# Optimization experiments

Measured on AMD Instinct MI355X. Metric: run time of the kernel, lower is better.

Reference implementation:

```python
import jax, jax.numpy as jnp
import numpy as np

ETA = 1.0
C_STAB = 0.1
SIGMA2 = 512.0  # RBF bandwidth, kernel_args['sigma2']
N_SAMPLE, S, D = 8192, 64, 512


def rbf_kernel(x, sigma2):
    # K[i,j] = exp(-||x_i - x_j||^2 / (2*sigma2)); x: [n, d] -> K: [n, n]
    sq = jnp.sum(x * x, axis=1)
    d2 = sq[:, None] + sq[None, :] - 2.0 * (x @ x.T)
    return jnp.exp(-d2 / (2.0 * sigma2))


def setup_inputs() -> dict:
    key = jax.random.key(0)
    k1, k2, k3 = jax.random.split(key, 3)
    return {
        "input_data": jax.random.normal(k1, (N_SAMPLE, D), dtype=jnp.float32),
        "weight": jax.random.normal(k2, (N_SAMPLE, S), dtype=jnp.float32),
        "inv_lambda_diag": jax.random.normal(k3, (S,), dtype=jnp.float32),
    }


def reference(input_data, weight, inv_lambda_diag):
    K = rbf_kernel(input_data, SIGMA2)          # [n, n]
    E = weight.T @ K                             # [s, n] : e_j for all samples at once
    # loss1 = sum_i e_i^T diag(inv_lambda) e_i, scaled
    loss1 = -jnp.sum(inv_lambda_diag[:, None] * E * E) / (2.0 * ETA ** 2)
    # loss2 = trace(W^T K W) = sum_{s,n} E[s,n] * W[n,s]
    loss2 = jnp.einsum("sn,ns->", E, weight) / (2.0 * ETA)
    L = loss1 + loss2
    return L + (C_STAB / 2.0) * jnp.square(L)
```

## Files before the change

kernel.cpp:

```cpp
#include <hip/hip_runtime.h>
#include <hip/hip_bf16.h>

typedef __bf16 bf16x8 __attribute__((ext_vector_type(8)));
typedef float f32x4 __attribute__((ext_vector_type(4)));
typedef long longx2 __attribute__((ext_vector_type(2)));

#define N 8192
#define D 512
#define NS 64

#define XS_OFF 0
#define WT_OFF (4 * 1024 * 1024)
#define SQ_OFF (WT_OFF + 1024 * 1024)
#define E_OFF  (SQ_OFF + 32 * 1024)
#define SC_OFF (E_OFF + N * NS * 4)

__global__ __launch_bounds__(256) void prep_x(const float* __restrict__ X,
                                              unsigned char* __restrict__ Xs,
                                              float* __restrict__ sq) {
    int row = blockIdx.x * 4 + (threadIdx.x >> 6);
    int l = threadIdx.x & 63;
    const float* src = X + (size_t)row * D + l * 8;
    float4 v0 = *(const float4*)src;
    float4 v1 = *(const float4*)(src + 4);
    int w0 = __builtin_amdgcn_cvt_pk_fp8_f32(v0.x, v0.y, 0, false);
    w0     = __builtin_amdgcn_cvt_pk_fp8_f32(v0.z, v0.w, w0, true);
    int w1 = __builtin_amdgcn_cvt_pk_fp8_f32(v1.x, v1.y, 0, false);
    w1     = __builtin_amdgcn_cvt_pk_fp8_f32(v1.z, v1.w, w1, true);
    int g = l >> 3, kh = (l >> 2) & 1, q = l & 3;
    int pos = g * 64 + ((q ^ (row & 3)) << 4) + (kh << 3);
    uint2 pk = make_uint2((unsigned)w0, (unsigned)w1);
    *(uint2*)(Xs + (size_t)row * 512 + pos) = pk;
    float acc = v0.x*v0.x + v0.y*v0.y + v0.z*v0.z + v0.w*v0.w
              + v1.x*v1.x + v1.y*v1.y + v1.z*v1.z + v1.w*v1.w;
    for (int off = 32; off > 0; off >>= 1) acc += __shfl_down(acc, off);
    if (l == 0) sq[row] = acc;
}

__global__ __launch_bounds__(256) void prep_w(const float* __restrict__ W,
                                              __bf16* __restrict__ WTs) {
    __shared__ float T[64][65];
    int i0 = blockIdx.x * 64;
    int t = threadIdx.x;
    for (int j = 0; j < 16; ++j) {
        int idx = t + 256 * j;
        int r = idx >> 6;
        int c = idx & 63;
        T[c][r] = W[(size_t)(i0 + r) * NS + c];
    }
    __syncthreads();
    for (int h = 0; h < 2; ++h)
        for (int j = 0; j < 8; ++j) {
            int idx = t + 256 * j;
            int s = idx >> 5, il = idx & 31;
            WTs[(size_t)(blockIdx.x * 2 + h) * 2048 + idx] = (__bf16)T[s][h * 32 + il];
        }
}

__global__ __launch_bounds__(256, 2) void kpca_main(
        const unsigned char* __restrict__ Xs, const __bf16* __restrict__ WTs,
        const float* __restrict__ sq, float* __restrict__ Eg) {
    __shared__ __align__(16) unsigned char U[34816];
    __shared__ __align__(16) __bf16 WT[8192];
    __shared__ __align__(16) float sqI[128];

    unsigned char* Xi = U;
    unsigned char* Xn = U + 8192;
    __bf16* KT = (__bf16*)U;

    const int t = threadIdx.x;
    const int w = t >> 6, l = t & 63;
    const int quad = l >> 4, l15 = l & 15;
    const int wm = w >> 1, wn = w & 1;
    const int n0 = blockIdx.x * 128;
    const int ic0 = blockIdx.y * 1024;
    const int fro = (quad ^ (l15 & 3)) << 4;

    float sqn_v[4];
    for (int nt = 0; nt < 4; ++nt)
        sqn_v[nt] = sq[n0 + wn * 64 + nt * 16 + l15];

    f32x4 accE[4][2];
    for (int st = 0; st < 4; ++st)
        for (int n2 = 0; n2 < 2; ++n2)
            accE[st][n2] = (f32x4){0.f, 0.f, 0.f, 0.f};

    const int c0 = t, c1 = t + 256;
    const int r0 = c0 >> 2, b0 = (c0 & 3) * 16;
    const int r1 = c1 >> 2, b1 = (c1 & 3) * 16;

    for (int it = 0; it < 8; ++it) {
        const int i0 = ic0 + it * 128;

        uint4 wv[4];
        const char* wb = (const char*)(WTs + (size_t)(i0 >> 5) * 2048);
        for (int j = 0; j < 4; ++j)
            wv[j] = *(const uint4*)(wb + (t + 256 * j) * 16);
        __syncthreads();
        for (int j = 0; j < 4; ++j)
            *(uint4*)((char*)WT + (t + 256 * j) * 16) = wv[j];
        if (t < 128) sqI[t] = sq[i0 + t];

        f32x4 accG[4][4];
        for (int mt = 0; mt < 4; ++mt)
            for (int nt = 0; nt < 4; ++nt)
                accG[mt][nt] = (f32x4){0.f, 0.f, 0.f, 0.f};

        for (int kc8 = 0; kc8 < 8; ++kc8) {
            const int kc = kc8 * 64;
            uint4 xi0 = *(const uint4*)(Xs + (size_t)(i0 + r0) * 512 + kc + b0);
            uint4 xi1 = *(const uint4*)(Xs + (size_t)(i0 + r1) * 512 + kc + b1);
            uint4 xn0 = *(const uint4*)(Xs + (size_t)(n0 + r0) * 512 + kc + b0);
            uint4 xn1 = *(const uint4*)(Xs + (size_t)(n0 + r1) * 512 + kc + b1);
            if (kc8) __syncthreads();
            *(uint4*)(Xi + c0 * 16) = xi0;
            *(uint4*)(Xi + c1 * 16) = xi1;
            *(uint4*)(Xn + c0 * 16) = xn0;
            *(uint4*)(Xn + c1 * 16) = xn1;
            __syncthreads();
            longx2 a[4], b[4];
            for (int mt = 0; mt < 4; ++mt)
                a[mt] = *(const longx2*)(Xi + (wm * 64 + mt * 16 + l15) * 64 + fro);
            for (int nt = 0; nt < 4; ++nt)
                b[nt] = *(const longx2*)(Xn + (wn * 64 + nt * 16 + l15) * 64 + fro);
            for (int mt = 0; mt < 4; ++mt)
                for (int nt = 0; nt < 4; ++nt)
                    accG[mt][nt] = __builtin_amdgcn_mfma_f32_16x16x32_fp8_fp8(
                        a[mt][0], b[nt][0], accG[mt][nt], 0, 0, 0);
            for (int mt = 0; mt < 4; ++mt)
                for (int nt = 0; nt < 4; ++nt)
                    accG[mt][nt] = __builtin_amdgcn_mfma_f32_16x16x32_fp8_fp8(
                        a[mt][1], b[nt][1], accG[mt][nt], 0, 0, 0);
        }
        __syncthreads();

        for (int mt = 0; mt < 4; ++mt) {
            int ibase = wm * 64 + mt * 16 + quad * 4;
            f32x4 si = *(const f32x4*)&sqI[ibase];
            for (int nt = 0; nt < 4; ++nt) {
                int nloc = wn * 64 + nt * 16 + l15;
                float sn = sqn_v[nt];
                union { __bf16 h[4]; uint2 u; } pk;
                for (int r = 0; r < 4; ++r) {
                    float d2 = si[r] + sn - 2.0f * accG[mt][nt][r];
                    pk.h[r] = (__bf16)__expf(d2 * -9.765625e-4f);
                }
                *(uint2*)(KT + nloc * 136 + ibase) = pk.u;
            }
        }
        __syncthreads();

        for (int kc2 = 0; kc2 < 4; ++kc2) {
            bf16x8 aw[4], bk[2];
            for (int st = 0; st < 4; ++st)
                aw[st] = *(const bf16x8*)(WT + kc2 * 2048 + (st * 16 + l15) * 32 + quad * 8);
            for (int n2 = 0; n2 < 2; ++n2)
                bk[n2] = *(const bf16x8*)(KT + (w * 32 + n2 * 16 + l15) * 136 + kc2 * 32 + quad * 8);
            for (int st = 0; st < 4; ++st)
                for (int n2 = 0; n2 < 2; ++n2)
                    accE[st][n2] = __builtin_amdgcn_mfma_f32_16x16x32_bf16(
                        aw[st], bk[n2], accE[st][n2], 0, 0, 0);
        }
    }

    for (int st = 0; st < 4; ++st)
        for (int n2 = 0; n2 < 2; ++n2)
            for (int r = 0; r < 4; ++r) {
                int s = st * 16 + quad * 4 + r;
                int n = n0 + w * 32 + n2 * 16 + l15;
                atomicAdd(Eg + (size_t)s * N + n, accE[st][n2][r]);
            }
}

__global__ __launch_bounds__(256) void loss_kernel(const float* __restrict__ Eg,
                                                   const float* __restrict__ W,
                                                   const float* __restrict__ lam,
                                                   float* __restrict__ Sacc) {
    int s = blockIdx.x;
    int t = threadIdx.x;
    float a1 = 0.f, a2 = 0.f;
    for (int n = t; n < N; n += 256) {
        float e = Eg[(size_t)s * N + n];
        a1 += e * e;
        a2 += e * W[(size_t)n * NS + s];
    }
    for (int off = 32; off > 0; off >>= 1) {
        a1 += __shfl_down(a1, off);
        a2 += __shfl_down(a2, off);
    }
    __shared__ float r1[4], r2[4];
    int wv = t >> 6, ln = t & 63;
    if (ln == 0) { r1[wv] = a1; r2[wv] = a2; }
    __syncthreads();
    if (t == 0) {
        atomicAdd(Sacc + 0, lam[s] * (r1[0] + r1[1] + r1[2] + r1[3]));
        atomicAdd(Sacc + 1, r2[0] + r2[1] + r2[2] + r2[3]);
    }
}

__global__ void finalize(const float* __restrict__ Sacc, float* __restrict__ out) {
    float L = 0.5f * (Sacc[1] - Sacc[0]);
    out[0] = L + 0.05f * L * L;
}

extern "C" void kernel_launch(void* const* d_in, const int* in_sizes, int n_in,
                              void* d_out, int out_size, void* d_ws, size_t ws_size,
                              hipStream_t stream) {
    const float* X   = (const float*)d_in[0];
    const float* W   = (const float*)d_in[1];
    const float* lam = (const float*)d_in[2];
    float* out = (float*)d_out;
    char* ws = (char*)d_ws;
    unsigned char* Xs = (unsigned char*)(ws + XS_OFF);
    __bf16* WTs = (__bf16*)(ws + WT_OFF);
    float* sq   = (float*)(ws + SQ_OFF);
    float* Eg   = (float*)(ws + E_OFF);
    float* Sacc = (float*)(ws + SC_OFF);

    hipMemsetAsync(Eg, 0, (size_t)N * NS * 4 + 8, stream);
    prep_x<<<N / 4, 256, 0, stream>>>(X, Xs, sq);
    prep_w<<<N / 64, 256, 0, stream>>>(W, WTs);
    kpca_main<<<dim3(64, 8), 256, 0, stream>>>(Xs, WTs, sq, Eg);
    loss_kernel<<<NS, 256, 0, stream>>>(Eg, W, lam, Sacc);
    finalize<<<1, 1, 0, stream>>>(Sacc, out);
}
```

Baseline: 178.2 us.

## Load fp8 MFMA operands directly from global, merge prep kernels, widen loss kernel

```diff
diff --git a/kernel.cpp b/kernel.cpp
--- a/kernel.cpp
+++ b/kernel.cpp
@@ -15,58 +15,53 @@
 #define E_OFF  (SQ_OFF + 32 * 1024)
 #define SC_OFF (E_OFF + N * NS * 4)
 
-__global__ __launch_bounds__(256) void prep_x(const float* __restrict__ X,
-                                              unsigned char* __restrict__ Xs,
-                                              float* __restrict__ sq) {
-    int row = blockIdx.x * 4 + (threadIdx.x >> 6);
-    int l = threadIdx.x & 63;
-    const float* src = X + (size_t)row * D + l * 8;
-    float4 v0 = *(const float4*)src;
-    float4 v1 = *(const float4*)(src + 4);
-    int w0 = __builtin_amdgcn_cvt_pk_fp8_f32(v0.x, v0.y, 0, false);
-    w0     = __builtin_amdgcn_cvt_pk_fp8_f32(v0.z, v0.w, w0, true);
-    int w1 = __builtin_amdgcn_cvt_pk_fp8_f32(v1.x, v1.y, 0, false);
-    w1     = __builtin_amdgcn_cvt_pk_fp8_f32(v1.z, v1.w, w1, true);
-    int g = l >> 3, kh = (l >> 2) & 1, q = l & 3;
-    int pos = g * 64 + ((q ^ (row & 3)) << 4) + (kh << 3);
-    uint2 pk = make_uint2((unsigned)w0, (unsigned)w1);
-    *(uint2*)(Xs + (size_t)row * 512 + pos) = pk;
-    float acc = v0.x*v0.x + v0.y*v0.y + v0.z*v0.z + v0.w*v0.w
-              + v1.x*v1.x + v1.y*v1.y + v1.z*v1.z + v1.w*v1.w;
-    for (int off = 32; off > 0; off >>= 1) acc += __shfl_down(acc, off);
-    if (l == 0) sq[row] = acc;
-}
-
-__global__ __launch_bounds__(256) void prep_w(const float* __restrict__ W,
-                                              __bf16* __restrict__ WTs) {
+__global__ __launch_bounds__(256) void prep(const float* __restrict__ X,
+                                            const float* __restrict__ W,
+                                            unsigned char* __restrict__ Xs,
+                                            float* __restrict__ sq,
+                                            __bf16* __restrict__ WTs) {
     __shared__ float T[64][65];
-    int i0 = blockIdx.x * 64;
     int t = threadIdx.x;
-    for (int j = 0; j < 16; ++j) {
-        int idx = t + 256 * j;
-        int r = idx >> 6;
-        int c = idx & 63;
-        T[c][r] = W[(size_t)(i0 + r) * NS + c];
-    }
-    __syncthreads();
-    for (int h = 0; h < 2; ++h)
-        for (int j = 0; j < 8; ++j) {
+    if (blockIdx.x < 2048) {
+        int row = blockIdx.x * 4 + (t >> 6);
+        int l = t & 63;
+        const float* src = X + (size_t)row * D + l * 8;
+        float4 v0 = *(const float4*)src;
+        float4 v1 = *(const float4*)(src + 4);
+        int w0 = __builtin_amdgcn_cvt_pk_fp8_f32(v0.x, v0.y, 0, false);
+        w0     = __builtin_amdgcn_cvt_pk_fp8_f32(v0.z, v0.w, w0, true);
+        int w1 = __builtin_amdgcn_cvt_pk_fp8_f32(v1.x, v1.y, 0, false);
+        w1     = __builtin_amdgcn_cvt_pk_fp8_f32(v1.z, v1.w, w1, true);
+        int g = l >> 3, kh = (l >> 2) & 1, q = l & 3;
+        int pos = g * 64 + q * 16 + kh * 8;
+        uint2 pk = make_uint2((unsigned)w0, (unsigned)w1);
+        *(uint2*)(Xs + (size_t)row * 512 + pos) = pk;
+        float acc = v0.x*v0.x + v0.y*v0.y + v0.z*v0.z + v0.w*v0.w
+                  + v1.x*v1.x + v1.y*v1.y + v1.z*v1.z + v1.w*v1.w;
+        for (int off = 32; off > 0; off >>= 1) acc += __shfl_down(acc, off);
+        if (l == 0) sq[row] = acc;
+    } else {
+        int i0 = (blockIdx.x - 2048) * 64;
+        for (int j = 0; j < 16; ++j) {
             int idx = t + 256 * j;
-            int s = idx >> 5, il = idx & 31;
-            WTs[(size_t)(blockIdx.x * 2 + h) * 2048 + idx] = (__bf16)T[s][h * 32 + il];
-        }
+            int r = idx >> 6;
+            int c = idx & 63;
+            T[c][r] = W[(size_t)(i0 + r) * NS + c];
+        }
+        __syncthreads();
+        for (int h = 0; h < 2; ++h)
+            for (int j = 0; j < 8; ++j) {
+                int idx = t + 256 * j;
+                int s = idx >> 5, il = idx & 31;
+                WTs[(size_t)((i0 >> 5) + h) * 2048 + idx] = (__bf16)T[s][h * 32 + il];
+            }
+    }
 }
 
 __global__ __launch_bounds__(256, 2) void kpca_main(
         const unsigned char* __restrict__ Xs, const __bf16* __restrict__ WTs,
         const float* __restrict__ sq, float* __restrict__ Eg) {
-    __shared__ __align__(16) unsigned char U[34816];
-    __shared__ __align__(16) __bf16 WT[8192];
-    __shared__ __align__(16) float sqI[128];
-
-    unsigned char* Xi = U;
-    unsigned char* Xn = U + 8192;
-    __bf16* KT = (__bf16*)U;
+    __shared__ __align__(16) __bf16 KT[128 * 136];
 
     const int t = threadIdx.x;
     const int w = t >> 6, l = t & 63;
@@ -74,55 +69,35 @@
     const int wm = w >> 1, wn = w & 1;
     const int n0 = blockIdx.x * 128;
     const int ic0 = blockIdx.y * 1024;
-    const int fro = (quad ^ (l15 & 3)) << 4;
 
     float sqn_v[4];
     for (int nt = 0; nt < 4; ++nt)
         sqn_v[nt] = sq[n0 + wn * 64 + nt * 16 + l15];
+
+    const unsigned char* Bb = Xs + (size_t)(n0 + wn * 64 + l15) * 512 + quad * 16;
 
     f32x4 accE[4][2];
     for (int st = 0; st < 4; ++st)
         for (int n2 = 0; n2 < 2; ++n2)
             accE[st][n2] = (f32x4){0.f, 0.f, 0.f, 0.f};
 
-    const int c0 = t, c1 = t + 256;
-    const int r0 = c0 >> 2, b0 = (c0 & 3) * 16;
-    const int r1 = c1 >> 2, b1 = (c1 & 3) * 16;
-
     for (int it = 0; it < 8; ++it) {
         const int i0 = ic0 + it * 128;
-
-        uint4 wv[4];
-        const char* wb = (const char*)(WTs + (size_t)(i0 >> 5) * 2048);
-        for (int j = 0; j < 4; ++j)
-            wv[j] = *(const uint4*)(wb + (t + 256 * j) * 16);
-        __syncthreads();
-        for (int j = 0; j < 4; ++j)
-            *(uint4*)((char*)WT + (t + 256 * j) * 16) = wv[j];
-        if (t < 128) sqI[t] = sq[i0 + t];
+        const unsigned char* Ab = Xs + (size_t)(i0 + wm * 64 + l15) * 512 + quad * 16;
 
         f32x4 accG[4][4];
         for (int mt = 0; mt < 4; ++mt)
             for (int nt = 0; nt < 4; ++nt)
                 accG[mt][nt] = (f32x4){0.f, 0.f, 0.f, 0.f};
 
+        #pragma unroll
         for (int kc8 = 0; kc8 < 8; ++kc8) {
             const int kc = kc8 * 64;
-            uint4 xi0 = *(const uint4*)(Xs + (size_t)(i0 + r0) * 512 + kc + b0);
-            uint4 xi1 = *(const uint4*)(Xs + (size_t)(i0 + r1) * 512 + kc + b1);
-            uint4 xn0 = *(const uint4*)(Xs + (size_t)(n0 + r0) * 512 + kc + b0);
-            uint4 xn1 = *(const uint4*)(Xs + (size_t)(n0 + r1) * 512 + kc + b1);
-            if (kc8) __syncthreads();
-            *(uint4*)(Xi + c0 * 16) = xi0;
-            *(uint4*)(Xi + c1 * 16) = xi1;
-            *(uint4*)(Xn + c0 * 16) = xn0;
-            *(uint4*)(Xn + c1 * 16) = xn1;
-            __syncthreads();
             longx2 a[4], b[4];
             for (int mt = 0; mt < 4; ++mt)
-                a[mt] = *(const longx2*)(Xi + (wm * 64 + mt * 16 + l15) * 64 + fro);
+                a[mt] = *(const longx2*)(Ab + mt * (16 * 512) + kc);
             for (int nt = 0; nt < 4; ++nt)
-                b[nt] = *(const longx2*)(Xn + (wn * 64 + nt * 16 + l15) * 64 + fro);
+                b[nt] = *(const longx2*)(Bb + nt * (16 * 512) + kc);
             for (int mt = 0; mt < 4; ++mt)
                 for (int nt = 0; nt < 4; ++nt)
                     accG[mt][nt] = __builtin_amdgcn_mfma_f32_16x16x32_fp8_fp8(
@@ -132,11 +107,21 @@
                     accG[mt][nt] = __builtin_amdgcn_mfma_f32_16x16x32_fp8_fp8(
                         a[mt][1], b[nt][1], accG[mt][nt], 0, 0, 0);
         }
+
+        bf16x8 aw[4][4];
+        {
+            const __bf16* wslab = WTs + (size_t)(i0 >> 5) * 2048;
+            for (int kc2 = 0; kc2 < 4; ++kc2)
+                for (int st = 0; st < 4; ++st)
+                    aw[kc2][st] = *(const bf16x8*)(wslab + kc2 * 2048 +
+                                                   (st * 16 + l15) * 32 + quad * 8);
+        }
+
         __syncthreads();
 
         for (int mt = 0; mt < 4; ++mt) {
             int ibase = wm * 64 + mt * 16 + quad * 4;
-            f32x4 si = *(const f32x4*)&sqI[ibase];
+            f32x4 si = *(const f32x4*)(sq + i0 + ibase);
             for (int nt = 0; nt < 4; ++nt) {
                 int nloc = wn * 64 + nt * 16 + l15;
                 float sn = sqn_v[nt];
@@ -151,15 +136,14 @@
         __syncthreads();
 
         for (int kc2 = 0; kc2 < 4; ++kc2) {
-            bf16x8 aw[4], bk[2];
-            for (int st = 0; st < 4; ++st)
-                aw[st] = *(const bf16x8*)(WT + kc2 * 2048 + (st * 16 + l15) * 32 + quad * 8);
+            bf16x8 bk[2];
             for (int n2 = 0; n2 < 2; ++n2)
-                bk[n2] = *(const bf16x8*)(KT + (w * 32 + n2 * 16 + l15) * 136 + kc2 * 32 + quad * 8);
+                bk[n2] = *(const bf16x8*)(KT + (w * 32 + n2 * 16 + l15) * 136 +
+                                          kc2 * 32 + quad * 8);
             for (int st = 0; st < 4; ++st)
                 for (int n2 = 0; n2 < 2; ++n2)
                     accE[st][n2] = __builtin_amdgcn_mfma_f32_16x16x32_bf16(
-                        aw[st], bk[n2], accE[st][n2], 0, 0, 0);
+                        aw[kc2][st], bk[n2], accE[st][n2], 0, 0, 0);
         }
     }
 
@@ -173,16 +157,18 @@
 }
 
 __global__ __launch_bounds__(256) void loss_kernel(const float* __restrict__ Eg,
-                                                   const float* __restrict__ W,
+                                                   const __bf16* __restrict__ WTs,
                                                    const float* __restrict__ lam,
                                                    float* __restrict__ Sacc) {
-    int s = blockIdx.x;
+    int s = blockIdx.x >> 2;
+    int nb = (blockIdx.x & 3) * 2048;
     int t = threadIdx.x;
     float a1 = 0.f, a2 = 0.f;
-    for (int n = t; n < N; n += 256) {
+    for (int j = 0; j < 8; ++j) {
+        int n = nb + t + j * 256;
         float e = Eg[(size_t)s * N + n];
         a1 += e * e;
-        a2 += e * W[(size_t)n * NS + s];
+        a2 += e * (float)WTs[(size_t)(n >> 5) * 2048 + s * 32 + (n & 31)];
     }
     for (int off = 32; off > 0; off >>= 1) {
         a1 += __shfl_down(a1, off);
@@ -218,9 +204,8 @@
     float* Sacc = (float*)(ws + SC_OFF);
 
     hipMemsetAsync(Eg, 0, (size_t)N * NS * 4 + 8, stream);
-    prep_x<<<N / 4, 256, 0, stream>>>(X, Xs, sq);
-    prep_w<<<N / 64, 256, 0, stream>>>(W, WTs);
+    prep<<<2048 + 128, 256, 0, stream>>>(X, W, Xs, sq, WTs);
     kpca_main<<<dim3(64, 8), 256, 0, stream>>>(Xs, WTs, sq, Eg);
-    loss_kernel<<<NS, 256, 0, stream>>>(Eg, W, lam, Sacc);
+    loss_kernel<<<256, 256, 0, stream>>>(Eg, WTs, lam, Sacc);
     finalize<<<1, 1, 0, stream>>>(Sacc, out);
 }
```

New measurement: 226.9 us. +27.3%, slower.
